# Kernel optimization log

Measured on AMD Instinct MI355X. Metric: run time of the kernel, lower is better.

## Reference

```python
import jax, jax.numpy as jnp
import numpy as np

NUM_USERS = 100000
NUM_ITEMS = 50000
EMBED_DIM = 64
NUM_LAYERS = 3
NUM_EDGES = 1250000
N = NUM_USERS + NUM_ITEMS


def setup_inputs() -> dict:
    key = jax.random.key(0)
    k1, k2, k3 = jax.random.split(key, 3)
    edge_index = jax.random.randint(k1, (2, NUM_EDGES), 0, N, dtype=jnp.int64)
    # nn.init.normal_(std=0.1)
    user_weight = 0.1 * jax.random.normal(k2, (NUM_USERS, EMBED_DIM), dtype=jnp.float32)
    item_weight = 0.1 * jax.random.normal(k3, (NUM_ITEMS, EMBED_DIM), dtype=jnp.float32)
    return {"edge_index": edge_index, "user_weight": user_weight, "item_weight": item_weight}


def reference(edge_index, user_weight, item_weight):
    src = edge_index[0]  # [E]
    dst = edge_index[1]  # [E]
    # degrees counted from dst column only (matches the torch loop)
    deg = jax.ops.segment_sum(jnp.ones_like(src, dtype=jnp.float32), dst, num_segments=N)
    norm = 1.0 / (jnp.sqrt(deg[src]) * jnp.sqrt(deg[dst]))  # [E]
    norm = jnp.where(jnp.isfinite(norm), norm, 0.0)

    emb = jnp.concatenate([user_weight, item_weight], axis=0)  # [N, D]
    acc = emb  # running sum over layer outputs (incl. layer 0)
    cur = emb
    for _ in range(NUM_LAYERS):
        msgs = cur[src] * norm[:, None]  # [E, D]
        cur = jax.ops.segment_sum(msgs, dst, num_segments=N)
        acc = acc + cur
    all_embeddings = acc / (NUM_LAYERS + 1)
    user_embeddings = all_embeddings[:NUM_USERS]
    item_embeddings = all_embeddings[NUM_USERS:]
    return all_embeddings, user_embeddings, item_embeddings
```

## Files before the change

### kernel.cpp

```cpp
#include <hip/hip_runtime.h>


#define NU 100000
#define NI 50000
#define NN 150000
#define DIM 64
#define NE 1250000
#define NF (NN * DIM)
#define NF4 (NF / 4)
#define SLOT 40
#define NBK 293
#define BSTRIDE 5120
#define PB 256
#define EPB ((NE + PB - 1) / PB)
#define CB ((NF4 + 255) / 256)

typedef unsigned short ushort_t;

__device__ inline ushort_t f2bf(float f) {
    unsigned u = __float_as_uint(f);
    return (ushort_t)((u + 0x7FFF + ((u >> 16) & 1)) >> 16);
}
__device__ inline float bf2f(ushort_t h) {
    return __uint_as_float(((unsigned)h) << 16);
}

__global__ void phaseA_kernel(const int* __restrict__ src, const int* __restrict__ dst,
                              int* __restrict__ bcursor, int2* __restrict__ part,
                              const float4* __restrict__ uw, const float4* __restrict__ iw,
                              ushort_t* __restrict__ embb) {
    int b = blockIdx.x;
    if (b < PB) {
        __shared__ int hist[NBK];
        __shared__ int cur[NBK];
        for (int i = threadIdx.x; i < NBK; i += 256) hist[i] = 0;
        __syncthreads();
        int e0 = b * EPB;
        int e1 = min(e0 + EPB, NE);
        for (int e = e0 + threadIdx.x; e < e1; e += 256)
            atomicAdd(&hist[dst[e] >> 9], 1);
        __syncthreads();
        for (int i = threadIdx.x; i < NBK; i += 256) {
            int h = hist[i];
            int base = h ? atomicAdd(&bcursor[i], h) : 0;
            cur[i] = i * BSTRIDE + base;
        }
        __syncthreads();
        for (int e = e0 + threadIdx.x; e < e1; e += 256) {
            int d = dst[e];
            int s = src[e];
            int p = atomicAdd(&cur[d >> 9], 1);
            part[p] = make_int2(s, d);
        }
    } else {
        int i = (b - PB) * 256 + threadIdx.x;
        if (i < NF4) {
            float4 v = (i < (NU * DIM) / 4) ? uw[i] : iw[i - (NU * DIM) / 4];
            ushort4 h;
            h.x = f2bf(v.x); h.y = f2bf(v.y); h.z = f2bf(v.z); h.w = f2bf(v.w);
            *(ushort4*)(embb + i * 4) = h;
        }
    }
}

__global__ void __launch_bounds__(256) phaseB_kernel(const int* __restrict__ bcursor,
                                                     const int2* __restrict__ part,
                                                     int* __restrict__ cursor,
                                                     float* __restrict__ rdeg,
                                                     int* __restrict__ slots) {
    __shared__ int dcount[512];
    int b = blockIdx.x;
    int cnt = min(bcursor[b], BSTRIDE);
    int nodebase = b * 512;
    for (int i = threadIdx.x; i < 512; i += 256) dcount[i] = 0;
    __syncthreads();
    const int2* pb = part + b * BSTRIDE;
    for (int i = threadIdx.x; i < cnt; i += 256) {
        int2 e = pb[i];
        int dloc = e.y - nodebase;
        int p = atomicAdd(&dcount[dloc], 1);
        slots[(nodebase + dloc) * SLOT + p] = e.x;
    }
    __syncthreads();
    for (int j = threadIdx.x; j < 512; j += 256) {
        int n = nodebase + j;
        if (n < NN) {
            int c = dcount[j];
            cursor[n] = c;
            rdeg[n] = (c > 0) ? rsqrtf((float)c) : 0.0f;
        }
    }
}

template <int LAYER>
__global__ void gather_kernel(const int* __restrict__ cursor, const float* __restrict__ rdeg,
                              const int* __restrict__ slots, const ushort_t* __restrict__ cur,
                              const float* __restrict__ uw, const float* __restrict__ iw,
                              float* __restrict__ acc, ushort_t* __restrict__ nxt) {
    int n = blockIdx.x * 4 + (threadIdx.x >> 6);
    int lane = threadIdx.x & 63;
    int dg = __builtin_amdgcn_readfirstlane(cursor[n]);
    float rd = __uint_as_float(__builtin_amdgcn_readfirstlane(__float_as_uint(rdeg[n])));
    const int* sb = slots + __builtin_amdgcn_readfirstlane(n * SLOT);
    float a = 0.0f;

#define EDGE(SV, I)                                                            \
    {                                                                          \
        int sv = (rem > (I)) ? (SV) : 0;                                       \
        float rw = rdeg[sv];                                                   \
        float w = (rem > (I)) ? rd * rw : 0.0f;                                \
        a = fmaf(w, bf2f(cur[sv * DIM + lane]), a);                            \
    }

    for (int c = 0; c < dg; c += 16) {
        const int* qb = sb + c;
        int rem = dg - c;
        int s0 = qb[0], s1 = qb[1], s2 = qb[2], s3 = qb[3];
        EDGE(s0, 0) EDGE(s1, 1) EDGE(s2, 2) EDGE(s3, 3)
        if (rem > 4) {
            int s4 = qb[4], s5 = qb[5], s6 = qb[6], s7 = qb[7];
            EDGE(s4, 4) EDGE(s5, 5) EDGE(s6, 6) EDGE(s7, 7)
        }
        if (rem > 8) {
            int s8 = qb[8], s9 = qb[9], s10 = qb[10], s11 = qb[11];
            EDGE(s8, 8) EDGE(s9, 9) EDGE(s10, 10) EDGE(s11, 11)
        }
        if (rem > 12) {
            int s12 = qb[12], s13 = qb[13], s14 = qb[14], s15 = qb[15];
            EDGE(s12, 12) EDGE(s13, 13) EDGE(s14, 14) EDGE(s15, 15)
        }
    }
#undef EDGE

    int idx = n * DIM + lane;
    if (LAYER == 1) {
        float e = (n < NU) ? uw[n * DIM + lane] : iw[(n - NU) * DIM + lane];
        acc[idx] = e + a;
        nxt[idx] = f2bf(a);
    } else if (LAYER == 2) {
        acc[idx] += a;
        nxt[idx] = f2bf(a);
    } else {
        float v = (acc[idx] + a) * 0.25f;
        acc[idx] = v;
        acc[NF + idx] = v;
    }
}

extern "C" void kernel_launch(void* const* d_in, const int* in_sizes, int n_in,
                              void* d_out, int out_size, void* d_ws, size_t ws_size,
                              hipStream_t stream) {
    const int* edge = (const int*)d_in[0];
    const int* src = edge;
    const int* dst = edge + NE;
    const float* uw = (const float*)d_in[1];
    const float* iw = (const float*)d_in[2];
    float* out = (float*)d_out;

    int* cursor    = (int*)d_ws;
    float* rdeg    = (float*)(cursor + NN);
    int* bcursor   = (int*)(rdeg + NN);
    int* slots     = bcursor + 320;
    int2* part     = (int2*)(slots + NN * SLOT);
    ushort_t* embb = (ushort_t*)(part + NBK * BSTRIDE);
    ushort_t* bufA = embb;
    ushort_t* bufT = (ushort_t*)(out + NF);

    const int B = 256;

    hipMemsetAsync(bcursor, 0, NBK * sizeof(int), stream);
    phaseA_kernel<<<PB + CB, B, 0, stream>>>(src, dst, bcursor, part,
                                             (const float4*)uw, (const float4*)iw, embb);
    phaseB_kernel<<<NBK, B, 0, stream>>>(bcursor, part, cursor, rdeg, slots);

    gather_kernel<1><<<NN / 4, B, 0, stream>>>(cursor, rdeg, slots, embb, uw, iw, out, bufT);
    gather_kernel<2><<<NN / 4, B, 0, stream>>>(cursor, rdeg, slots, bufT, uw, iw, out, bufA);
    gather_kernel<3><<<NN / 4, B, 0, stream>>>(cursor, rdeg, slots, bufA, uw, iw, out, nullptr);
}
```

Before: 331.9 us.

## Pre-scale features by source degree and gather four edges per wavefront

The per-edge rdeg[src] load goes away because each layer stores bf16 features already multiplied by the source node's inverse square-root degree. Phase B now produces the initial scaled embedding. In the gather, each wavefront handles four edges at once: each 16-lane group reads a full 128-byte row as uint2 (4 bf16 values per lane), and the partial sums are combined with xor shuffles. Setup kernels move to 1024-thread blocks. The trade-offs are an extra rounding step (rd applied before bf16 conversion) and three-quarters of lanes sitting idle during the final stores.

```diff
diff --git a/kernel.cpp b/kernel.cpp
--- a/kernel.cpp
+++ b/kernel.cpp
@@ -13,7 +13,6 @@
 #define BSTRIDE 5120
 #define PB 256
 #define EPB ((NE + PB - 1) / PB)
-#define CB ((NF4 + 255) / 256)
 
 typedef unsigned short ushort_t;
 
@@ -21,129 +20,162 @@
     unsigned u = __float_as_uint(f);
     return (ushort_t)((u + 0x7FFF + ((u >> 16) & 1)) >> 16);
 }
-__device__ inline float bf2f(ushort_t h) {
-    return __uint_as_float(((unsigned)h) << 16);
-}
-
-__global__ void phaseA_kernel(const int* __restrict__ src, const int* __restrict__ dst,
-                              int* __restrict__ bcursor, int2* __restrict__ part,
-                              const float4* __restrict__ uw, const float4* __restrict__ iw,
-                              ushort_t* __restrict__ embb) {
+__device__ inline float bflo(unsigned u) { return __uint_as_float(u << 16); }
+__device__ inline float bfhi(unsigned u) { return __uint_as_float(u & 0xffff0000u); }
+
+__global__ void __launch_bounds__(1024) phaseA_kernel(const int* __restrict__ src,
+                                                      const int* __restrict__ dst,
+                                                      int* __restrict__ bcursor,
+                                                      int2* __restrict__ part) {
+    __shared__ int hist[NBK];
+    __shared__ int cur[NBK];
     int b = blockIdx.x;
-    if (b < PB) {
-        __shared__ int hist[NBK];
-        __shared__ int cur[NBK];
-        for (int i = threadIdx.x; i < NBK; i += 256) hist[i] = 0;
-        __syncthreads();
-        int e0 = b * EPB;
-        int e1 = min(e0 + EPB, NE);
-        for (int e = e0 + threadIdx.x; e < e1; e += 256)
-            atomicAdd(&hist[dst[e] >> 9], 1);
-        __syncthreads();
-        for (int i = threadIdx.x; i < NBK; i += 256) {
-            int h = hist[i];
-            int base = h ? atomicAdd(&bcursor[i], h) : 0;
-            cur[i] = i * BSTRIDE + base;
-        }
-        __syncthreads();
-        for (int e = e0 + threadIdx.x; e < e1; e += 256) {
-            int d = dst[e];
-            int s = src[e];
-            int p = atomicAdd(&cur[d >> 9], 1);
-            part[p] = make_int2(s, d);
-        }
-    } else {
-        int i = (b - PB) * 256 + threadIdx.x;
-        if (i < NF4) {
-            float4 v = (i < (NU * DIM) / 4) ? uw[i] : iw[i - (NU * DIM) / 4];
-            ushort4 h;
-            h.x = f2bf(v.x); h.y = f2bf(v.y); h.z = f2bf(v.z); h.w = f2bf(v.w);
-            *(ushort4*)(embb + i * 4) = h;
-        }
-    }
-}
-
-__global__ void __launch_bounds__(256) phaseB_kernel(const int* __restrict__ bcursor,
-                                                     const int2* __restrict__ part,
-                                                     int* __restrict__ cursor,
-                                                     float* __restrict__ rdeg,
-                                                     int* __restrict__ slots) {
+    int tid = threadIdx.x;
+    if (tid < NBK) hist[tid] = 0;
+    __syncthreads();
+    int e0 = b * EPB;
+    int e1 = min(e0 + EPB, NE);
+    for (int e = e0 + tid; e < e1; e += 1024)
+        atomicAdd(&hist[dst[e] >> 9], 1);
+    __syncthreads();
+    if (tid < NBK) {
+        int h = hist[tid];
+        int base = h ? atomicAdd(&bcursor[tid], h) : 0;
+        cur[tid] = tid * BSTRIDE + base;
+    }
+    __syncthreads();
+    for (int e = e0 + tid; e < e1; e += 1024) {
+        int d = dst[e];
+        int s = src[e];
+        int p = atomicAdd(&cur[d >> 9], 1);
+        part[p] = make_int2(s, d);
+    }
+}
+
+__global__ void __launch_bounds__(1024) phaseB_kernel(const int* __restrict__ bcursor,
+                                                      const int2* __restrict__ part,
+                                                      int* __restrict__ cursor,
+                                                      float* __restrict__ rdeg,
+                                                      int* __restrict__ slots,
+                                                      const float4* __restrict__ uw4,
+                                                      const float4* __restrict__ iw4,
+                                                      ushort_t* __restrict__ embb) {
     __shared__ int dcount[512];
+    __shared__ float rfs[512];
     int b = blockIdx.x;
+    int tid = threadIdx.x;
     int cnt = min(bcursor[b], BSTRIDE);
     int nodebase = b * 512;
-    for (int i = threadIdx.x; i < 512; i += 256) dcount[i] = 0;
+    if (tid < 512) dcount[tid] = 0;
     __syncthreads();
     const int2* pb = part + b * BSTRIDE;
-    for (int i = threadIdx.x; i < cnt; i += 256) {
+    for (int i = tid; i < cnt; i += 1024) {
         int2 e = pb[i];
         int dloc = e.y - nodebase;
         int p = atomicAdd(&dcount[dloc], 1);
         slots[(nodebase + dloc) * SLOT + p] = e.x;
     }
     __syncthreads();
-    for (int j = threadIdx.x; j < 512; j += 256) {
-        int n = nodebase + j;
+    if (tid < 512) {
+        int n = nodebase + tid;
+        float r = 0.0f;
         if (n < NN) {
-            int c = dcount[j];
+            int c = dcount[tid];
             cursor[n] = c;
-            rdeg[n] = (c > 0) ? rsqrtf((float)c) : 0.0f;
+            r = (c > 0) ? rsqrtf((float)c) : 0.0f;
+            rdeg[n] = r;
         }
+        rfs[tid] = r;
+    }
+    __syncthreads();
+    int nnode = min(512, NN - nodebase);
+    int lim = nnode * 16;
+    for (int q = tid; q < lim; q += 1024) {
+        int nl = q >> 4;
+        int node = nodebase + nl;
+        int c4 = q & 15;
+        float4 v = (node < NU) ? uw4[node * 16 + c4] : iw4[(node - NU) * 16 + c4];
+        float r = rfs[nl];
+        ushort4 h;
+        h.x = f2bf(v.x * r); h.y = f2bf(v.y * r);
+        h.z = f2bf(v.z * r); h.w = f2bf(v.w * r);
+        *(ushort4*)(embb + node * DIM + c4 * 4) = h;
     }
 }
 
 template <int LAYER>
-__global__ void gather_kernel(const int* __restrict__ cursor, const float* __restrict__ rdeg,
-                              const int* __restrict__ slots, const ushort_t* __restrict__ cur,
-                              const float* __restrict__ uw, const float* __restrict__ iw,
-                              float* __restrict__ acc, ushort_t* __restrict__ nxt) {
+__global__ void __launch_bounds__(256) gather_kernel(const int* __restrict__ cursor,
+                                                     const float* __restrict__ rdeg,
+                                                     const int* __restrict__ slots,
+                                                     const ushort_t* __restrict__ cur,
+                                                     const float4* __restrict__ uw4,
+                                                     const float4* __restrict__ iw4,
+                                                     float4* __restrict__ acc,
+                                                     ushort_t* __restrict__ nxt) {
     int n = blockIdx.x * 4 + (threadIdx.x >> 6);
     int lane = threadIdx.x & 63;
+    int j = lane >> 4;
+    int d = lane & 15;
+    bool j1 = (j & 1) != 0;
+    bool j2 = (j & 2) != 0;
     int dg = __builtin_amdgcn_readfirstlane(cursor[n]);
     float rd = __uint_as_float(__builtin_amdgcn_readfirstlane(__float_as_uint(rdeg[n])));
-    const int* sb = slots + __builtin_amdgcn_readfirstlane(n * SLOT);
-    float a = 0.0f;
-
-#define EDGE(SV, I)                                                            \
-    {                                                                          \
-        int sv = (rem > (I)) ? (SV) : 0;                                       \
-        float rw = rdeg[sv];                                                   \
-        float w = (rem > (I)) ? rd * rw : 0.0f;                                \
-        a = fmaf(w, bf2f(cur[sv * DIM + lane]), a);                            \
-    }
-
-    for (int c = 0; c < dg; c += 16) {
-        const int* qb = sb + c;
-        int rem = dg - c;
-        int s0 = qb[0], s1 = qb[1], s2 = qb[2], s3 = qb[3];
-        EDGE(s0, 0) EDGE(s1, 1) EDGE(s2, 2) EDGE(s3, 3)
-        if (rem > 4) {
-            int s4 = qb[4], s5 = qb[5], s6 = qb[6], s7 = qb[7];
-            EDGE(s4, 4) EDGE(s5, 5) EDGE(s6, 6) EDGE(s7, 7)
+    const int* sb = slots + __builtin_amdgcn_readfirstlane(n) * SLOT;
+    float a0 = 0.0f, a1 = 0.0f, a2 = 0.0f, a3 = 0.0f;
+
+    for (int c = 0; c < dg; c += 8) {
+        int4 qa = *(const int4*)(sb + c);
+        int4 qb = *(const int4*)(sb + c + 4);
+        int ta = j1 ? qa.y : qa.x;
+        int tb = j1 ? qa.w : qa.z;
+        int sva = j2 ? tb : ta;
+        int tc = j1 ? qb.y : qb.x;
+        int td = j1 ? qb.w : qb.z;
+        int svb = j2 ? td : tc;
+        bool va = (c + j) < dg;
+        bool vb = (c + 4 + j) < dg;
+        sva = va ? sva : 0;
+        svb = vb ? svb : 0;
+        uint2 ua = *((const uint2*)(cur + sva * DIM) + d);
+        uint2 ub = *((const uint2*)(cur + svb * DIM) + d);
+        float wa = va ? 1.0f : 0.0f;
+        float wb = vb ? 1.0f : 0.0f;
+        a0 = fmaf(wa, bflo(ua.x), a0); a1 = fmaf(wa, bfhi(ua.x), a1);
+        a2 = fmaf(wa, bflo(ua.y), a2); a3 = fmaf(wa, bfhi(ua.y), a3);
+        a0 = fmaf(wb, bflo(ub.x), a0); a1 = fmaf(wb, bfhi(ub.x), a1);
+        a2 = fmaf(wb, bflo(ub.y), a2); a3 = fmaf(wb, bfhi(ub.y), a3);
+    }
+
+    a0 += __shfl_xor(a0, 16); a1 += __shfl_xor(a1, 16);
+    a2 += __shfl_xor(a2, 16); a3 += __shfl_xor(a3, 16);
+    a0 += __shfl_xor(a0, 32); a1 += __shfl_xor(a1, 32);
+    a2 += __shfl_xor(a2, 32); a3 += __shfl_xor(a3, 32);
+
+    float c0 = rd * a0, c1 = rd * a1, c2 = rd * a2, c3 = rd * a3;
+    int idx4 = n * 16 + d;
+
+    if (j == 0) {
+        if (LAYER == 1) {
+            float4 e = (n < NU) ? uw4[n * 16 + d] : iw4[(n - NU) * 16 + d];
+            acc[idx4] = make_float4(e.x + c0, e.y + c1, e.z + c2, e.w + c3);
+            ushort4 h;
+            h.x = f2bf(rd * c0); h.y = f2bf(rd * c1);
+            h.z = f2bf(rd * c2); h.w = f2bf(rd * c3);
+            *(ushort4*)(nxt + n * DIM + d * 4) = h;
+        } else if (LAYER == 2) {
+            float4 t = acc[idx4];
+            acc[idx4] = make_float4(t.x + c0, t.y + c1, t.z + c2, t.w + c3);
+            ushort4 h;
+            h.x = f2bf(rd * c0); h.y = f2bf(rd * c1);
+            h.z = f2bf(rd * c2); h.w = f2bf(rd * c3);
+            *(ushort4*)(nxt + n * DIM + d * 4) = h;
+        } else {
+            float4 t = acc[idx4];
+            float4 v = make_float4((t.x + c0) * 0.25f, (t.y + c1) * 0.25f,
+                                   (t.z + c2) * 0.25f, (t.w + c3) * 0.25f);
+            acc[idx4] = v;
+            acc[NF4 + idx4] = v;
         }
-        if (rem > 8) {
-            int s8 = qb[8], s9 = qb[9], s10 = qb[10], s11 = qb[11];
-            EDGE(s8, 8) EDGE(s9, 9) EDGE(s10, 10) EDGE(s11, 11)
-        }
-        if (rem > 12) {
-            int s12 = qb[12], s13 = qb[13], s14 = qb[14], s15 = qb[15];
-            EDGE(s12, 12) EDGE(s13, 13) EDGE(s14, 14) EDGE(s15, 15)
-        }
-    }
-#undef EDGE
-
-    int idx = n * DIM + lane;
-    if (LAYER == 1) {
-        float e = (n < NU) ? uw[n * DIM + lane] : iw[(n - NU) * DIM + lane];
-        acc[idx] = e + a;
-        nxt[idx] = f2bf(a);
-    } else if (LAYER == 2) {
-        acc[idx] += a;
-        nxt[idx] = f2bf(a);
-    } else {
-        float v = (acc[idx] + a) * 0.25f;
-        acc[idx] = v;
-        acc[NF + idx] = v;
     }
 }
 
@@ -166,14 +198,18 @@
     ushort_t* bufA = embb;
     ushort_t* bufT = (ushort_t*)(out + NF);
 
-    const int B = 256;
-
     hipMemsetAsync(bcursor, 0, NBK * sizeof(int), stream);
-    phaseA_kernel<<<PB + CB, B, 0, stream>>>(src, dst, bcursor, part,
-                                             (const float4*)uw, (const float4*)iw, embb);
-    phaseB_kernel<<<NBK, B, 0, stream>>>(bcursor, part, cursor, rdeg, slots);
-
-    gather_kernel<1><<<NN / 4, B, 0, stream>>>(cursor, rdeg, slots, embb, uw, iw, out, bufT);
-    gather_kernel<2><<<NN / 4, B, 0, stream>>>(cursor, rdeg, slots, bufT, uw, iw, out, bufA);
-    gather_kernel<3><<<NN / 4, B, 0, stream>>>(cursor, rdeg, slots, bufA, uw, iw, out, nullptr);
-}
+    phaseA_kernel<<<PB, 1024, 0, stream>>>(src, dst, bcursor, part);
+    phaseB_kernel<<<NBK, 1024, 0, stream>>>(bcursor, part, cursor, rdeg, slots,
+                                            (const float4*)uw, (const float4*)iw, embb);
+
+    gather_kernel<1><<<NN / 4, 256, 0, stream>>>(cursor, rdeg, slots, embb,
+                                                 (const float4*)uw, (const float4*)iw,
+                                                 (float4*)out, bufT);
+    gather_kernel<2><<<NN / 4, 256, 0, stream>>>(cursor, rdeg, slots, bufT,
+                                                 (const float4*)uw, (const float4*)iw,
+                                                 (float4*)out, bufA);
+    gather_kernel<3><<<NN / 4, 256, 0, stream>>>(cursor, rdeg, slots, bufA,
+                                                 (const float4*)uw, (const float4*)iw,
+                                                 (float4*)out, nullptr);
+}
```

Result: faster. 303.0 us (-8.7%).
